# Kernel optimization log

Hardware: AMD Instinct MI355X
Metric: run time of the kernel (lower is better)

## Reference

```python
import jax, jax.numpy as jnp
import numpy as np

GAMMA, ZETA = -0.1, 1.1
N_BITS = 4
QMAX = (1 << N_BITS) - 1  # 15
OUT, IN, D, K = 4096, 4096, 8, 4096
L = (OUT * IN) // D  # 2097152 blocks, no padding needed


def setup_inputs() -> dict:
    key = jax.random.key(0)
    k = jax.random.split(key, 7)
    x = jax.random.normal(k[0], (4, 2048, IN), jnp.float32)
    codebook = jax.random.normal(k[1], (K, D), jnp.float32)
    indices = jax.random.randint(k[2], (L,), 0, K, jnp.int32)
    base_int = jax.random.randint(k[3], (OUT, IN), 0, QMAX, jnp.int32)
    scale = jax.random.uniform(k[4], (OUT, 1), jnp.float32)
    zero = jax.random.uniform(k[5], (OUT, 1), jnp.float32)
    bias = jax.random.normal(k[6], (OUT,), jnp.float32)
    return {"x": x, "codebook": codebook, "indices": indices,
            "base_int": base_int, "scale": scale, "zero": zero, "bias": bias}


def reference(x, codebook, indices, base_int, scale, zero, bias):
    # Gather codebook blocks and rebuild alpha with the weight's shape [OUT, IN]
    alpha = codebook[indices].reshape(OUT, IN)
    # Rectified sigmoid (soft quant mode)
    r = jnp.clip(jax.nn.sigmoid(alpha) * (ZETA - GAMMA) + GAMMA, 0.0, 1.0)
    # Affine int-quant reconstruction
    q_int = jnp.clip(base_int.astype(scale.dtype) + r + zero, 0.0, float(QMAX))
    Wq = scale * (q_int - zero)  # [OUT, IN]
    # F.linear: x @ Wq^T + bias
    return jnp.einsum('bsi,oi->bso', x, Wq) + bias
```

## Files before the change

### kernel.cpp

```cpp
#include <hip/hip_runtime.h>

#define M_DIM 8192
#define N_DIM 4096
#define K_DIM 4096
#define L_BLK 2097152
#define K2 8192

typedef __attribute__((ext_vector_type(8))) short short8;
typedef __attribute__((ext_vector_type(8))) unsigned short ushort8;
typedef __attribute__((ext_vector_type(4))) float f32x4;

__device__ __forceinline__ unsigned short f2bf(float f) {
  unsigned int u = __float_as_uint(f);
  unsigned int r = (u + 0x7fffu + ((u >> 16) & 1u)) >> 16;
  return (unsigned short)r;
}

__device__ __forceinline__ void gld16(const void* g, void* l) {
  __builtin_amdgcn_global_load_lds(
      (const __attribute__((address_space(1))) void*)g,
      (__attribute__((address_space(3))) void*)l, 16, 0, 0);
}

__global__ void dequant_kernel(const float* __restrict__ cb,
                               const int* __restrict__ idx,
                               const int* __restrict__ base,
                               const float* __restrict__ scale,
                               const float* __restrict__ zero,
                               unsigned short* __restrict__ W) {
  const int b = blockIdx.x * 256 + threadIdx.x;
  const int o = b >> 9;
  const float s = scale[o];
  const float z = zero[o];
  const int ci = idx[b];
  const float4* crow = (const float4*)(cb + (size_t)ci * 8);
  float4 c0 = crow[0], c1 = crow[1];
  const int4* brow = (const int4*)(base + (size_t)b * 8);
  int4 b0 = brow[0], b1 = brow[1];
  float a[8]  = {c0.x, c0.y, c0.z, c0.w, c1.x, c1.y, c1.z, c1.w};
  int   bi[8] = {b0.x, b0.y, b0.z, b0.w, b1.x, b1.y, b1.z, b1.w};
  union { unsigned short h[8]; ushort8 v; } u;
#pragma unroll
  for (int d = 0; d < 8; ++d) {
    float sg = 1.0f / (1.0f + __expf(-a[d]));
    float r = fminf(fmaxf(sg * 1.2f - 0.1f, 0.0f), 1.0f);
    float q = fminf(fmaxf((float)bi[d] + r + z, 0.0f), 15.0f);
    u.h[d] = f2bf(s * (q - z));
  }
  *(ushort8*)(W + (size_t)b * 8) = u.v;
}

__global__ void xconv_kernel(const float* __restrict__ x,
                             unsigned short* __restrict__ xb) {
  const size_t i = (size_t)blockIdx.x * 256 + threadIdx.x;
  const float4* X = (const float4*)x;
  float4 a0 = X[i * 2], a1 = X[i * 2 + 1];
  float f[8] = {a0.x, a0.y, a0.z, a0.w, a1.x, a1.y, a1.z, a1.w};
  union { unsigned short h[8]; ushort8 v; } u;
#pragma unroll
  for (int d = 0; d < 8; ++d) u.h[d] = f2bf(f[d]);
  *(ushort8*)(xb + i * 8) = u.v;
}


#define VMW(N) asm volatile("s_waitcnt vmcnt(" #N ")" ::: "memory")
#define FENCE asm volatile("" ::: "memory")
#define BARM do { FENCE; __builtin_amdgcn_s_barrier(); FENCE; } while (0)

#define RDB(BF, BUFO) \
  _Pragma("unroll") for (int n = 0; n < 4; ++n) \
  _Pragma("unroll") for (int kk = 0; kk < 2; ++kk) \
    BF[n][kk] = *(const short8*)(lds + (BUFO) + 32768 + \
        (wn * 64 + n * 16 + r16) * 128 + (acol0 ^ (kk << 6)));

#define RDA(AF, BUFO, P) \
  _Pragma("unroll") for (int mi = 0; mi < 2; ++mi) \
  _Pragma("unroll") for (int kk = 0; kk < 2; ++kk) \
    AF[mi][kk] = *(const short8*)(lds + (BUFO) + \
        (wm * 128 + (2 * (P) + mi) * 16 + r16) * 128 + (acol0 ^ (kk << 6)));

#define FMQ(P, AF, BF) do { \
  __builtin_amdgcn_s_setprio(1); \
  __builtin_amdgcn_sched_barrier(0); \
  _Pragma("unroll") for (int kk = 0; kk < 2; ++kk) \
  _Pragma("unroll") for (int mi = 0; mi < 2; ++mi) \
  _Pragma("unroll") for (int n = 0; n < 4; ++n) \
    acc[2 * (P) + mi][n] = __builtin_amdgcn_mfma_f32_16x16x32_bf16( \
        AF[mi][kk], BF[n][kk], acc[2 * (P) + mi][n], 0, 0, 0); \
  __builtin_amdgcn_sched_barrier(0); \
  __builtin_amdgcn_s_setprio(0); \
} while (0)

#define STAGE6(NXT, KT) do { \
  stB(NXT, 0, KT); stB(NXT, 1, KT); stB(NXT, 2, KT); stB(NXT, 3, KT); \
  stA(NXT, 0, KT); stA(NXT, 2, KT); } while (0)
#define STAGE2(NXT, KT) do { stA(NXT, 1, KT); stA(NXT, 3, KT); } while (0)

#define ITER(BFC, BFN, CUR, NXT, KT) do { \
   \
  RDA(afB, CUR, 1); STAGE6(NXT, KT); FMQ(0, afA, BFC); VMW(6); BARM; \
   \
  RDA(afA, CUR, 2); STAGE2(NXT, KT); FMQ(1, afB, BFC); \
   \
  RDA(afB, CUR, 3); FMQ(2, afA, BFC); VMW(2); BARM; \
   \
  RDB(BFN, NXT); RDA(afA, NXT, 0); FMQ(3, afB, BFC); BARM; \
} while (0)

__global__ __launch_bounds__(512, 2)
void gemm_bt(const unsigned short* __restrict__ A,
             const unsigned short* __restrict__ B,
             const float* __restrict__ bias,
             float* __restrict__ C) {
  __shared__ char lds[131072];
  const int tid = threadIdx.x;
  const int lane = tid & 63;
  const int w = tid >> 6;
  const int wm = w >> 2;
  const int wn = w & 3;
  const int r16 = lane & 15;
  const int g = lane >> 4;
  const int acol0 = (g << 4) ^ ((r16 & 7) << 4);

  const int s = (int)blockIdx.x;
  const int wg = (s & 7) * 64 + (s >> 3);
  const int bm = wg & 31;
  const int bn = wg >> 5;

  const char* Abase = (const char*)A + (size_t)bm * 256 * K2;
  const char* Bbase = (const char*)B + (size_t)bn * 256 * K2;

  const int strow = tid >> 3;
  const int scol = ((tid & 7) * 16) ^ ((strow & 7) << 4);
  const int sdst = w * 1024;

  auto stA = [&](int bo, int c, int kt) {
    gld16(Abase + (size_t)(c * 64 + strow) * K2 + kt * 128 + scol,
          lds + bo + c * 8192 + sdst);
  };
  auto stB = [&](int bo, int c, int kt) {
    gld16(Bbase + (size_t)(c * 64 + strow) * K2 + kt * 128 + scol,
          lds + bo + 32768 + c * 8192 + sdst);
  };

  f32x4 acc[8][4] = {};
  short8 bfA[4][2], bfB[4][2];
  short8 afA[2][2], afB[2][2];

  STAGE6(0, 0); STAGE2(0, 0);
  VMW(0); BARM;
  RDB(bfA, 0); RDA(afA, 0, 0);

  for (int tp = 0; tp < 31; ++tp) {
    ITER(bfA, bfB, 0, 65536, 2 * tp + 1);
    ITER(bfB, bfA, 65536, 0, 2 * tp + 2);
  }
  ITER(bfA, bfB, 0, 65536, 63);
  RDA(afB, 65536, 1); FMQ(0, afA, bfB); VMW(0); BARM;
  RDA(afA, 65536, 2); FMQ(1, afB, bfB);
  RDA(afB, 65536, 3); FMQ(2, afA, bfB);
  FMQ(3, afB, bfB);

  FENCE;

  const int cb0 = bn * 256 + wn * 64 + r16;
  float bv[4];
#pragma unroll
  for (int n = 0; n < 4; ++n) bv[n] = bias[cb0 + n * 16];
#pragma unroll
  for (int m = 0; m < 8; ++m) {
#pragma unroll
    for (int j = 0; j < 4; ++j) {
      int row = bm * 256 + wm * 128 + m * 16 + g * 4 + j;
      float* Crow = C + (size_t)row * N_DIM + cb0;
#pragma unroll
      for (int n = 0; n < 4; ++n) Crow[n * 16] = acc[m][n][j] + bv[n];
    }
  }
}

extern "C" void kernel_launch(void* const* d_in, const int* in_sizes, int n_in,
                              void* d_out, int out_size, void* d_ws, size_t ws_size,
                              hipStream_t stream) {
  const float* x     = (const float*)d_in[0];
  const float* cb    = (const float*)d_in[1];
  const int*   idx   = (const int*)d_in[2];
  const int*   base  = (const int*)d_in[3];
  const float* scale = (const float*)d_in[4];
  const float* zero  = (const float*)d_in[5];
  const float* bias  = (const float*)d_in[6];
  float* out = (float*)d_out;

  unsigned short* Wq = (unsigned short*)d_ws;
  unsigned short* Xb = (unsigned short*)((char*)d_ws + (size_t)N_DIM * K_DIM * 2);

  dequant_kernel<<<L_BLK / 256, 256, 0, stream>>>(cb, idx, base, scale, zero, Wq);
  xconv_kernel<<<(M_DIM * K_DIM / 8) / 256, 256, 0, stream>>>(x, Xb);
  gemm_bt<<<(M_DIM / 256) * (N_DIM / 256), 512, 0, stream>>>(Xb, Wq, bias, out);
}
```

Baseline: 331.8 us.

## Restructure GEMM main loop into 8-barrier ping-pong with deeper prefetch

Rewrites the GEMM K-loop schedule. Global-to-LDS loads are now issued up to two tiles ahead, and part of the next tile's stores go into the buffer currently being consumed once its data has been read into registers. Each quarter-step is bracketed by barriers and an explicit lgkmcnt(0) wait, in the style of a ping-pong schedule between the two waves per SIMD. This is meant to hide global load latency better and keep the MFMA pipes fed, but it doubles the barrier count and serialises the LDS reads ahead of the MFMAs, which may add stalls.

```diff
diff --git a/kernel.cpp b/kernel.cpp
--- a/kernel.cpp
+++ b/kernel.cpp
@@ -65,7 +65,9 @@
 
 #define VMW(N) asm volatile("s_waitcnt vmcnt(" #N ")" ::: "memory")
 #define FENCE asm volatile("" ::: "memory")
-#define BARM do { FENCE; __builtin_amdgcn_s_barrier(); FENCE; } while (0)
+#define BAR do { FENCE; __builtin_amdgcn_s_barrier(); FENCE; } while (0)
+#define LGKM0 do { asm volatile("s_waitcnt lgkmcnt(0)" ::: "memory"); \
+                   __builtin_amdgcn_sched_barrier(0); } while (0)
 
 #define RDB(BF, BUFO) \
   _Pragma("unroll") for (int n = 0; n < 4; ++n) \
@@ -91,20 +93,18 @@
   __builtin_amdgcn_s_setprio(0); \
 } while (0)
 
-#define STAGE6(NXT, KT) do { \
-  stB(NXT, 0, KT); stB(NXT, 1, KT); stB(NXT, 2, KT); stB(NXT, 3, KT); \
-  stA(NXT, 0, KT); stA(NXT, 2, KT); } while (0)
-#define STAGE2(NXT, KT) do { stA(NXT, 1, KT); stA(NXT, 3, KT); } while (0)
-
-#define ITER(BFC, BFN, CUR, NXT, KT) do { \
-   \
-  RDA(afB, CUR, 1); STAGE6(NXT, KT); FMQ(0, afA, BFC); VMW(6); BARM; \
-   \
-  RDA(afA, CUR, 2); STAGE2(NXT, KT); FMQ(1, afB, BFC); \
-   \
-  RDA(afB, CUR, 3); FMQ(2, afA, BFC); VMW(2); BARM; \
-   \
-  RDB(BFN, NXT); RDA(afA, NXT, 0); FMQ(3, afB, BFC); BARM; \
+#define ITER(CUR, NXT, T) do { \
+   RDB(bf, CUR); RDA(afA, CUR, 0); \
+  stA(NXT, 2, (T) + 1); stA(NXT, 3, (T) + 1); \
+  BAR; LGKM0; FMQ(0, afA, bf); BAR; \
+   RDA(afA, CUR, 1); \
+  stB(CUR, 0, (T) + 2); stB(CUR, 1, (T) + 2); \
+  BAR; LGKM0; FMQ(1, afA, bf); BAR; \
+   RDA(afA, CUR, 2); RDA(afB, CUR, 3); \
+  stB(CUR, 2, (T) + 2); stB(CUR, 3, (T) + 2); \
+  BAR; LGKM0; FMQ(2, afA, bf); BAR; \
+   stA(CUR, 0, (T) + 2); stA(CUR, 1, (T) + 2); \
+  VMW(6); BAR; LGKM0; FMQ(3, afB, bf); BAR; \
 } while (0)
 
 __global__ __launch_bounds__(512, 2)
@@ -144,22 +144,34 @@
   };
 
   f32x4 acc[8][4] = {};
-  short8 bfA[4][2], bfB[4][2];
+  short8 bf[4][2];
   short8 afA[2][2], afB[2][2];
 
-  STAGE6(0, 0); STAGE2(0, 0);
-  VMW(0); BARM;
-  RDB(bfA, 0); RDA(afA, 0, 0);
+  stB(0, 0, 0); stB(0, 1, 0); stB(0, 2, 0); stB(0, 3, 0);
+  stA(0, 0, 0); stA(0, 1, 0); stA(0, 2, 0); stA(0, 3, 0);
+  stB(65536, 0, 1); stB(65536, 1, 1); stB(65536, 2, 1); stB(65536, 3, 1);
+  stA(65536, 0, 1); stA(65536, 1, 1);
+  VMW(6); BAR;
 
   for (int tp = 0; tp < 31; ++tp) {
-    ITER(bfA, bfB, 0, 65536, 2 * tp + 1);
-    ITER(bfB, bfA, 65536, 0, 2 * tp + 2);
+    ITER(0, 65536, 2 * tp);
+    ITER(65536, 0, 2 * tp + 1);
   }
-  ITER(bfA, bfB, 0, 65536, 63);
-  RDA(afB, 65536, 1); FMQ(0, afA, bfB); VMW(0); BARM;
-  RDA(afA, 65536, 2); FMQ(1, afB, bfB);
-  RDA(afB, 65536, 3); FMQ(2, afA, bfB);
-  FMQ(3, afB, bfB);
+  RDB(bf, 0); RDA(afA, 0, 0);
+  stA(65536, 2, 63); stA(65536, 3, 63);
+  BAR; LGKM0; FMQ(0, afA, bf); BAR;
+  RDA(afA, 0, 1);
+  BAR; LGKM0; FMQ(1, afA, bf); BAR;
+  RDA(afA, 0, 2); RDA(afB, 0, 3);
+  BAR; LGKM0; FMQ(2, afA, bf); BAR;
+  VMW(0); BAR; LGKM0; FMQ(3, afB, bf); BAR;
+  RDB(bf, 65536); RDA(afA, 65536, 0);
+  LGKM0; FMQ(0, afA, bf);
+  RDA(afA, 65536, 1);
+  LGKM0; FMQ(1, afA, bf);
+  RDA(afA, 65536, 2); RDA(afB, 65536, 3);
+  LGKM0; FMQ(2, afA, bf);
+  FMQ(3, afB, bf);
 
   FENCE;
 
```

Result: faster. 310.2 us (-6.5%).
